# Optimization experiments

Measured on AMD Instinct MI355X. Metric: run time of the kernel, lower is better.

Reference implementation:

```python
import jax, jax.numpy as jnp
import numpy as np

C = 64
CQK = C // 8  # query/key channels = 8


def setup_inputs() -> dict:
    key = jax.random.key(0)
    ks = jax.random.split(key, 7)
    B, D, H, W = 1, 16, 32, 32
    x = jax.random.normal(ks[0], (B, C, D, H, W), dtype=jnp.float32)
    # 1x1x1 Conv3d weights collapse to [out_ch, in_ch] matrices; std=0.01 per nn.init.normal_
    wq = 0.01 * jax.random.normal(ks[1], (CQK, C), dtype=jnp.float32)
    bq = jnp.zeros((CQK,), dtype=jnp.float32)
    wk = 0.01 * jax.random.normal(ks[2], (CQK, C), dtype=jnp.float32)
    bk = jnp.zeros((CQK,), dtype=jnp.float32)
    wv = 0.01 * jax.random.normal(ks[3], (C, C), dtype=jnp.float32)
    bv = jnp.zeros((C,), dtype=jnp.float32)
    gamma = jnp.zeros((1,), dtype=jnp.float32)  # nn.Parameter(torch.zeros(1))
    return {"x": x, "wq": wq, "bq": bq, "wk": wk, "bk": bk, "wv": wv, "bv": bv, "gamma": gamma}


def reference(x, wq, bq, wk, bk, wv, bv, gamma):
    B, Cc, D, H, W = x.shape
    N = D * H * W
    xf = x.reshape(B, Cc, N)  # [B, C, N]
    # 1x1x1 convs == per-position linear projections
    q = jnp.einsum('oc,bcn->bon', wq, xf) + bq[None, :, None]   # [B, CQK, N]
    k = jnp.einsum('oc,bcn->bon', wk, xf) + bk[None, :, None]   # [B, CQK, N]
    v = jnp.einsum('oc,bcn->bon', wv, xf) + bv[None, :, None]   # [B, C, N]
    # attention[b, i, j] = softmax_j( q[:, :, i] . k[:, :, j] )  -> [B, N, N]
    scores = jnp.einsum('bon,bom->bnm', q, k)
    attn = jax.nn.softmax(scores, axis=-1)
    # out[b, c, i] = sum_j v[b, c, j] * attn[b, i, j]
    out = jnp.einsum('bcm,bnm->bcn', v, attn).reshape(B, Cc, D, H, W)
    return x + gamma * out
```

## Files before the change

### kernel.cpp

```cpp
#include <hip/hip_runtime.h>

#define NPOS 16384
#define KSPLIT 8
#define KEYS_PER_BLK (NPOS / KSPLIT)
#define CHUNK 512
#define LOG2E 1.4426950408889634f

typedef short bf16x8 __attribute__((ext_vector_type(8)));
typedef unsigned short u16x8 __attribute__((ext_vector_type(8)));
typedef float floatx16 __attribute__((ext_vector_type(16)));
typedef float floatx2 __attribute__((ext_vector_type(2)));

static __device__ __forceinline__ unsigned short f2bf(float f) {
    return (unsigned short)(__builtin_bit_cast(unsigned int, f) >> 16);
}
static __device__ __forceinline__ float bf2f(unsigned short h) {
    return __builtin_bit_cast(float, (unsigned int)h << 16);
}

#if __has_builtin(__builtin_amdgcn_exp2f)
static __device__ __forceinline__ float exp2_fast(float x) {
    return __builtin_amdgcn_exp2f(x);
}
#else
static __device__ __forceinline__ float exp2_fast(float x) {
    float r;
    asm("v_exp_f32 %0, %1" : "=v"(r) : "v"(x));
    return r;
}
#endif

static __device__ __forceinline__ unsigned int pk_bf16(float e_even, float e_odd) {
    return __builtin_amdgcn_perm(__builtin_bit_cast(unsigned int, e_odd),
                                 __builtin_bit_cast(unsigned int, e_even),
                                 0x07060302u);
}

static __device__ __forceinline__ int sigma(int n) {
    const int w12 = n & 12;
    return (w12 == 4 || w12 == 8) ? (n ^ 12) : n;
}

__global__ __launch_bounds__(256) void proj_kernel(
    const float* __restrict__ x,
    const float* __restrict__ wq, const float* __restrict__ bq,
    const float* __restrict__ wk, const float* __restrict__ bk,
    const float* __restrict__ wv, const float* __restrict__ bv,
    unsigned short* __restrict__ qb16, unsigned short* __restrict__ kb16,
    unsigned short* __restrict__ vbg16)
{
    const int t = threadIdx.x;
    const int n = blockIdx.x * 256 + t;
    const int g = blockIdx.y;

    const float* w;
    const float* b;
    if (g == 0)      { w = wq; b = bq; }
    else if (g == 1) { w = wk; b = bk; }
    else             { w = wv + (g - 2) * 8 * 64; b = bv + (g - 2) * 8; }

    float acc[8];
#pragma unroll
    for (int oo = 0; oo < 8; ++oo) acc[oo] = b[oo];
#pragma unroll 16
    for (int c = 0; c < 64; ++c) {
        const float xv = x[c * NPOS + n];
#pragma unroll
        for (int oo = 0; oo < 8; ++oo)
            acc[oo] = fmaf(w[oo * 64 + c], xv, acc[oo]);
    }

    if (g == 0) {
        u16x8 qp;
#pragma unroll
        for (int j = 0; j < 8; ++j) qp[j] = f2bf(acc[j] * LOG2E);
        ((uint4*)qb16)[n] = __builtin_bit_cast(uint4, qp);
    } else if (g == 1) {
        u16x8 kp;
#pragma unroll
        for (int j = 0; j < 8; ++j) kp[j] = f2bf(acc[j]);
        ((uint4*)kb16)[n] = __builtin_bit_cast(uint4, kp);
    } else {
        const int o0 = (g - 2) * 8;
        const int np = sigma(n);
        const size_t base = (size_t)(np >> 3) * 512 + (np & 7);
#pragma unroll
        for (int oo = 0; oo < 8; ++oo)
            vbg16[base + (size_t)(o0 + oo) * 8] = f2bf(acc[oo]);
    }
}

__global__ __launch_bounds__(256, 6) void attn_kernel(
    const uint4* __restrict__ qb4,
    const uint4* __restrict__ kb4,
    const uint4* __restrict__ vbg4,
    unsigned short* __restrict__ nump,
    float* __restrict__ denp)
{
    __shared__ __align__(16) char smem[8448];
    uint4* k_lds = (uint4*)smem;

    const int t     = threadIdx.x;
    const int wave  = t >> 6;
    const int lane  = t & 63;
    const int m     = lane & 31;
    const int half  = lane >> 5;
    const int qhalf = wave >> 1;
    const int khalf = wave & 1;

    const int qblk = blockIdx.x >> 3;
    const int kq   = blockIdx.x & 7;
    const int i0   = qblk * 64;
    const int jb   = kq * KEYS_PER_BLK;

    if (t == 0) k_lds[512] = make_uint4(0, 0, 0, 0);

    uint4 qa4 = (half == 0) ? qb4[i0 + qhalf * 32 + m] : make_uint4(0, 0, 0, 0);
    const bf16x8 bqf = __builtin_bit_cast(bf16x8, qa4);

    floatx16 accA = {};
    floatx16 accB = {};
    floatx2  dacc2 = {0.f, 0.f};

#pragma unroll 1
    for (int c4 = 0; c4 < 4; ++c4) {
        const int j0 = jb + c4 * CHUNK;
        __syncthreads();
        k_lds[t]       = kb4[j0 + t];
        k_lds[256 + t] = kb4[j0 + 256 + t];
        __syncthreads();

        const int kwb = khalf * 256;
#pragma unroll 1
        for (int st = 0; st < 8; ++st) {
            const int kb_ = kwb + st * 32;
            const bf16x8 ak = __builtin_bit_cast(
                bf16x8, k_lds[half ? 512 : (kb_ + m)]);
            const floatx16 s = __builtin_amdgcn_mfma_f32_32x32x16_bf16(
                ak, bqf, (floatx16){}, 0, 0, 0);

            float e[16];
#pragma unroll
            for (int r = 0; r < 16; ++r) e[r] = exp2_fast(s[r]);
#pragma unroll
            for (int p = 0; p < 8; ++p)
                dacc2 += (floatx2){e[2 * p], e[2 * p + 1]};
            unsigned int P[8];
#pragma unroll
            for (int p = 0; p < 8; ++p) P[p] = pk_bf16(e[2 * p], e[2 * p + 1]);

            const int g8t = (j0 + kb_) >> 3;
#pragma unroll
            for (int f = 0; f < 2; ++f) {
                uint4 afu;
                afu.x = P[4 * f + 0];
                afu.y = P[4 * f + 1];
                afu.z = P[4 * f + 2];
                afu.w = P[4 * f + 3];
                const bf16x8 af = __builtin_bit_cast(bf16x8, afu);

                const int g8 = g8t + f * 2 + half;
                const bf16x8 v0 = __builtin_bit_cast(
                    bf16x8, vbg4[(size_t)g8 * 64 + m]);
                const bf16x8 v1 = __builtin_bit_cast(
                    bf16x8, vbg4[(size_t)g8 * 64 + 32 + m]);
                accA = __builtin_amdgcn_mfma_f32_32x32x16_bf16(af, v0, accA,
                                                               0, 0, 0);
                accB = __builtin_amdgcn_mfma_f32_32x32x16_bf16(af, v1, accB,
                                                               0, 0, 0);
            }
        }
    }

    const float dl = dacc2[0] + dacc2[1];
    const float dw = dl + __shfl_xor(dl, 32);

    __syncthreads();
    float*          xden = (float*)smem;
    unsigned short* xacc = (unsigned short*)(smem + 256);
    const int recl = qhalf * 64 + lane;
    if (khalf == 1) {
        if (half == 0) xden[qhalf * 32 + m] = dw;
        u16x8 a0, a1, a2, a3;
#pragma unroll
        for (int j = 0; j < 8; ++j) {
            a0[j] = f2bf(accA[j]);
            a1[j] = f2bf(accA[8 + j]);
            a2[j] = f2bf(accB[j]);
            a3[j] = f2bf(accB[8 + j]);
        }
        uint4* dst = (uint4*)(xacc + recl * 32);
        dst[0] = __builtin_bit_cast(uint4, a0);
        dst[1] = __builtin_bit_cast(uint4, a1);
        dst[2] = __builtin_bit_cast(uint4, a2);
        dst[3] = __builtin_bit_cast(uint4, a3);
    }
    __syncthreads();
    if (khalf == 0) {
        const uint4* src = (const uint4*)(xacc + recl * 32);
        const u16x8 b0 = __builtin_bit_cast(u16x8, src[0]);
        const u16x8 b1 = __builtin_bit_cast(u16x8, src[1]);
        const u16x8 b2 = __builtin_bit_cast(u16x8, src[2]);
        const u16x8 b3 = __builtin_bit_cast(u16x8, src[3]);
        u16x8 o0, o1, o2, o3;
#pragma unroll
        for (int j = 0; j < 8; ++j) {
            o0[j] = f2bf(accA[j]      + bf2f(b0[j]));
            o1[j] = f2bf(accA[8 + j]  + bf2f(b1[j]));
            o2[j] = f2bf(accB[j]      + bf2f(b2[j]));
            o3[j] = f2bf(accB[8 + j]  + bf2f(b3[j]));
        }
        const size_t base =
            ((((size_t)kq * 256 + qblk) * 2 + qhalf) * 64 + lane) * 32;
        uint4* gdst = (uint4*)(nump + base);
        gdst[0] = __builtin_bit_cast(uint4, o0);
        gdst[1] = __builtin_bit_cast(uint4, o1);
        gdst[2] = __builtin_bit_cast(uint4, o2);
        gdst[3] = __builtin_bit_cast(uint4, o3);
        if (half == 0)
            denp[(size_t)kq * NPOS + i0 + qhalf * 32 + m] =
                dw + xden[qhalf * 32 + m];
    }
}

__global__ __launch_bounds__(256) void finalize_kernel(
    const float* __restrict__ x,
    const unsigned short* __restrict__ nump,
    const float* __restrict__ denp,
    const float* __restrict__ gamma,
    float* __restrict__ out)
{
    const int b    = blockIdx.x;
    const int qblk = b >> 1;
    const int qh   = b & 1;
    const int t    = threadIdx.x;
    const int lane = t >> 2;
    const int u    = t & 3;
    const int n0   = qblk * 64 + qh * 32;

    __shared__ float dsum[32];
    if (t < 32) dsum[t] = 0.f;
    __syncthreads();
    atomicAdd(&dsum[t & 31], denp[(size_t)(t >> 5) * NPOS + n0 + (t & 31)]);
    __syncthreads();

    float ns[8];
#pragma unroll
    for (int j = 0; j < 8; ++j) ns[j] = 0.f;
#pragma unroll
    for (int kq = 0; kq < 8; ++kq) {
        const size_t base =
            ((((size_t)kq * 256 + qblk) * 2 + qh) * 64 + lane) * 32 + u * 8;
        const u16x8 h = __builtin_bit_cast(u16x8, *(const uint4*)(nump + base));
#pragma unroll
        for (int j = 0; j < 8; ++j) ns[j] += bf2f(h[j]);
    }

    const float g     = gamma[0];
    const int   clow  = lane & 31;
    const int   hf    = lane >> 5;
    const int   chigh = u >> 1;
    const int   c     = chigh * 32 + clow;
#pragma unroll
    for (int j = 0; j < 8; ++j) {
        const int off = u * 8 + j;
        const int r   = off & 15;
        const int row = (r & 3) + 8 * (r >> 2) + 4 * hf;
        const int n   = n0 + row;
        const size_t gi = (size_t)c * NPOS + n;
        out[gi] = fmaf(g, ns[j] * __builtin_amdgcn_rcpf(dsum[row]), x[gi]);
    }
}

extern "C" void kernel_launch(void* const* d_in, const int* in_sizes, int n_in,
                              void* d_out, int out_size, void* d_ws, size_t ws_size,
                              hipStream_t stream)
{
    (void)in_sizes; (void)n_in; (void)out_size; (void)ws_size;

    const float* x     = (const float*)d_in[0];
    const float* wq    = (const float*)d_in[1];
    const float* bq    = (const float*)d_in[2];
    const float* wk    = (const float*)d_in[3];
    const float* bk    = (const float*)d_in[4];
    const float* wv    = (const float*)d_in[5];
    const float* bv    = (const float*)d_in[6];
    const float* gamma = (const float*)d_in[7];
    float* out = (float*)d_out;

    char* ws = (char*)d_ws;
    unsigned short* qb16  = (unsigned short*)(ws);
    unsigned short* kb16  = (unsigned short*)(ws + 262144);
    unsigned short* vbg16 = (unsigned short*)(ws + 524288);
    unsigned short* nump  = (unsigned short*)(ws + 2621440);
    float*          denp  = (float*)(ws + 19398656);

    proj_kernel<<<dim3(NPOS / 256, 10), 256, 0, stream>>>(
        x, wq, bq, wk, bk, wv, bv, qb16, kb16, vbg16);
    attn_kernel<<<(NPOS / 64) * KSPLIT, 256, 0, stream>>>(
        (const uint4*)qb16, (const uint4*)kb16, (const uint4*)vbg16,
        nump, denp);
    finalize_kernel<<<512, 256, 0, stream>>>(x, nump, denp, gamma, out);
}
```

Measured before the change: 141.4 us.

## Lower attn occupancy target, unroll key loop, transpose finalize output via LDS

The attention kernel's launch-bounds occupancy hint drops from 6 to 4 waves, giving the compiler more registers. The key-step loop is unrolled by 2, the denominator is accumulated in two independent registers, and the zero-padded LDS slot for the upper half-wave's K operand is removed so every lane reads real key data. The finalize kernel now stages the numerators through a padded LDS tile so global reads of x and writes of out are contiguous along positions. The tradeoffs are lower occupancy for better ILP, and the removed zero padding may change the MFMA result for half-waves that relied on zeros.

```diff
diff --git a/kernel.cpp b/kernel.cpp
--- a/kernel.cpp
+++ b/kernel.cpp
@@ -90,7 +90,7 @@
     }
 }
 
-__global__ __launch_bounds__(256, 6) void attn_kernel(
+__global__ __launch_bounds__(256, 4) void attn_kernel(
     const uint4* __restrict__ qb4,
     const uint4* __restrict__ kb4,
     const uint4* __restrict__ vbg4,
@@ -113,14 +113,14 @@
     const int i0   = qblk * 64;
     const int jb   = kq * KEYS_PER_BLK;
 
-    if (t == 0) k_lds[512] = make_uint4(0, 0, 0, 0);
-
     uint4 qa4 = (half == 0) ? qb4[i0 + qhalf * 32 + m] : make_uint4(0, 0, 0, 0);
     const bf16x8 bqf = __builtin_bit_cast(bf16x8, qa4);
 
     floatx16 accA = {};
     floatx16 accB = {};
-    floatx2  dacc2 = {0.f, 0.f};
+    floatx2  dacc[2];
+    dacc[0] = (floatx2){0.f, 0.f};
+    dacc[1] = (floatx2){0.f, 0.f};
 
 #pragma unroll 1
     for (int c4 = 0; c4 < 4; ++c4) {
@@ -131,11 +131,10 @@
         __syncthreads();
 
         const int kwb = khalf * 256;
-#pragma unroll 1
+#pragma unroll 2
         for (int st = 0; st < 8; ++st) {
             const int kb_ = kwb + st * 32;
-            const bf16x8 ak = __builtin_bit_cast(
-                bf16x8, k_lds[half ? 512 : (kb_ + m)]);
+            const bf16x8 ak = __builtin_bit_cast(bf16x8, k_lds[kb_ + m]);
             const floatx16 s = __builtin_amdgcn_mfma_f32_32x32x16_bf16(
                 ak, bqf, (floatx16){}, 0, 0, 0);
 
@@ -144,7 +143,7 @@
             for (int r = 0; r < 16; ++r) e[r] = exp2_fast(s[r]);
 #pragma unroll
             for (int p = 0; p < 8; ++p)
-                dacc2 += (floatx2){e[2 * p], e[2 * p + 1]};
+                dacc[p & 1] += (floatx2){e[2 * p], e[2 * p + 1]};
             unsigned int P[8];
 #pragma unroll
             for (int p = 0; p < 8; ++p) P[p] = pk_bf16(e[2 * p], e[2 * p + 1]);
@@ -172,7 +171,8 @@
         }
     }
 
-    const float dl = dacc2[0] + dacc2[1];
+    const floatx2 dfold = dacc[0] + dacc[1];
+    const float dl = dfold[0] + dfold[1];
     const float dw = dl + __shfl_xor(dl, 32);
 
     __syncthreads();
@@ -239,10 +239,10 @@
     const int n0   = qblk * 64 + qh * 32;
 
     __shared__ float dsum[32];
+    __shared__ float ot[32 * 66];
     if (t < 32) dsum[t] = 0.f;
     __syncthreads();
     atomicAdd(&dsum[t & 31], denp[(size_t)(t >> 5) * NPOS + n0 + (t & 31)]);
-    __syncthreads();
 
     float ns[8];
 #pragma unroll
@@ -256,19 +256,28 @@
         for (int j = 0; j < 8; ++j) ns[j] += bf2f(h[j]);
     }
 
-    const float g     = gamma[0];
-    const int   clow  = lane & 31;
-    const int   hf    = lane >> 5;
-    const int   chigh = u >> 1;
-    const int   c     = chigh * 32 + clow;
+    const int clow = lane & 31;
+    const int hf   = lane >> 5;
 #pragma unroll
     for (int j = 0; j < 8; ++j) {
         const int off = u * 8 + j;
         const int r   = off & 15;
         const int row = (r & 3) + 8 * (r >> 2) + 4 * hf;
-        const int n   = n0 + row;
-        const size_t gi = (size_t)c * NPOS + n;
-        out[gi] = fmaf(g, ns[j] * __builtin_amdgcn_rcpf(dsum[row]), x[gi]);
+        const int c   = (off >> 4) * 32 + clow;
+        ot[row * 66 + c] = ns[j];
+    }
+    __syncthreads();
+
+    const float g  = gamma[0];
+    const int   c2 = t >> 2;
+    const int   nq = t & 3;
+    const int   nb = nq * 8;
+#pragma unroll
+    for (int j = 0; j < 8; ++j) {
+        const int row = nb + j;
+        const size_t gi = (size_t)c2 * NPOS + n0 + row;
+        out[gi] = fmaf(g, ot[row * 66 + c2] *
+                              __builtin_amdgcn_rcpf(dsum[row]), x[gi]);
     }
 }
 
```

Measured after the change: 138.0 us. 2.4% less time.
